# Optimization experiments

Hardware: AMD Instinct MI355X
Metric: run time of the kernel (lower is better)

The kernel has to match this reference:

```python
import jax, jax.numpy as jnp
import numpy as np

# Structure constants T[k, p, q] = sign such that (a (x) b)_k = sum_{p,q} T[k,p,q] a_p b_q,
# transcribed term-by-term from clifford_product_3d (Cl(3,0), metric +,+,+).
_TERMS = [
    (0,0,0, 1),(0,1,1, 1),(0,2,2, 1),(0,3,3, 1),(0,4,4,-1),(0,5,5,-1),(0,6,6,-1),(0,7,7,-1),
    (1,0,1, 1),(1,1,0, 1),(1,2,4,-1),(1,3,5, 1),(1,4,2, 1),(1,5,3,-1),(1,6,7,-1),(1,7,6,-1),
    (2,0,2, 1),(2,1,4, 1),(2,2,0, 1),(2,3,6,-1),(2,4,1,-1),(2,5,7, 1),(2,6,3, 1),(2,7,5,-1),
    (3,0,3, 1),(3,1,5,-1),(3,2,6, 1),(3,3,0, 1),(3,4,7,-1),(3,5,1,-1),(3,6,2,-1),(3,7,4, 1),
    (4,0,4, 1),(4,1,2, 1),(4,2,1,-1),(4,3,7, 1),(4,4,0, 1),(4,5,6,-1),(4,6,5, 1),(4,7,3,-1),
    (5,0,5, 1),(5,1,3,-1),(5,2,7, 1),(5,3,1, 1),(5,4,6, 1),(5,5,0, 1),(5,6,4,-1),(5,7,2,-1),
    (6,0,6, 1),(6,1,7,-1),(6,2,3,-1),(6,3,2, 1),(6,4,5,-1),(6,5,4, 1),(6,6,0, 1),(6,7,1, 1),
    (7,0,7, 1),(7,1,6, 1),(7,2,5,-1),(7,3,4, 1),(7,4,3, 1),(7,5,2,-1),(7,6,1, 1),(7,7,0, 1),
]

def _clifford_table():
    T = np.zeros((8, 8, 8), dtype=np.float32)
    for k, p, q, s in _TERMS:
        T[k, p, q] = s
    return jnp.asarray(T)

_T = _clifford_table()


def setup_inputs() -> dict:
    key = jax.random.key(0)
    k1, k2 = jax.random.split(key)
    C_in, C_out = 8, 8
    x = jax.random.normal(k1, (4096, 512, C_in, 8), dtype=jnp.float32)
    weight = jax.random.normal(k2, (C_out, C_in, 8), dtype=jnp.float32) * C_in ** (-0.5)
    bias = jnp.zeros((C_out, 8), dtype=jnp.float32)
    return {"x": x, "weight": weight, "bias": bias}


def reference(x, weight, bias):
    # out[..., o, k] = sum_i sum_{p,q} T[k,p,q] * weight[o,i,p] * x[..., i, q] + bias[o,k]
    # Contract weight with T first (tiny), then a single GEMM-like contraction over (i,q):
    # avoids the naive [..., C_out, C_in, 8] broadcast intermediate entirely.
    wT = jnp.einsum('kpq,oip->oikq', _T.astype(weight.dtype), weight)  # [C_out, C_in, 8, 8]
    out = jnp.einsum('oikq,biq->bok', wT, x.reshape(-1, *x.shape[-2:]))
    out = out.reshape(*x.shape[:-2], *out.shape[-2:])
    return out + bias
```

## Files before the change

kernel.cpp:

```cpp
#include <hip/hip_runtime.h>
#include <stdint.h>

__constant__ signed char QTAB[64] = {
    0,1,2,3,4,5,6,7,
    1,0,4,5,2,3,7,6,
    2,4,0,6,1,7,3,5,
    3,5,6,0,7,1,2,4,
    4,2,1,7,0,6,5,3,
    5,3,7,1,6,0,4,2,
    6,7,3,2,5,4,0,1,
    7,6,5,4,3,2,1,0};
__constant__ signed char SGN[64] = {
    1, 1, 1, 1,-1,-1,-1,-1,
    1, 1,-1, 1, 1,-1,-1,-1,
    1, 1, 1,-1,-1, 1, 1,-1,
    1,-1, 1, 1,-1,-1,-1, 1,
    1, 1,-1, 1, 1,-1, 1,-1,
    1,-1, 1, 1, 1, 1,-1,-1,
    1,-1,-1, 1,-1, 1, 1, 1,
    1, 1,-1, 1, 1,-1, 1, 1};

__global__ void clifford_prep(const float* __restrict__ weight,
                              float* __restrict__ W2) {
    int t = threadIdx.x;
    for (int e = t; e < 4096; e += 256) {
        int o = e >> 9, i = (e >> 6) & 7, k = (e >> 3) & 7, p = e & 7;
        int q = (int)QTAB[k * 8 + p];
        float s = (float)SGN[k * 8 + p];
        W2[((i * 8 + q) * 64) + (o * 8 + k)] = s * weight[(o * 8 + i) * 8 + p];
    }
}

#define LSTR 33

__global__ __launch_bounds__(256) void clifford_main(
    const float* __restrict__ x, const float* __restrict__ W,
    const float* __restrict__ bias, float* __restrict__ out, int nB) {
    __shared__ float lds[4][64 * LSTR];
    const int wave = threadIdx.x >> 6;
    const int lane = threadIdx.x & 63;
    float* Lw = lds[wave];
    const long long base = ((long long)blockIdx.x * 4 + wave) * 64;
    if (base >= nB) return;
    const float* xt = x + base * 64;
    float* ot = out + base * 64;
    const int r8 = lane >> 3;
    const int c8 = (lane & 7) * 4;

    float4 r0[8];
#pragma unroll
    for (int i = 0; i < 8; ++i)
        r0[i] = *(const float4*)(xt + (size_t)(r8 + 8 * i) * 64 + c8);
#pragma unroll
    for (int i = 0; i < 8; ++i) {
        int b = r8 + 8 * i;
        Lw[b * LSTR + c8 + 0] = r0[i].x;
        Lw[b * LSTR + c8 + 1] = r0[i].y;
        Lw[b * LSTR + c8 + 2] = r0[i].z;
        Lw[b * LSTR + c8 + 3] = r0[i].w;
    }

    float4 r1[8];
#pragma unroll
    for (int i = 0; i < 8; ++i)
        r1[i] = *(const float4*)(xt + (size_t)(r8 + 8 * i) * 64 + 32 + c8);

    float acc[64];
#pragma unroll
    for (int m = 0; m < 64; ++m) acc[m] = bias[m];

#pragma unroll 2
    for (int iq = 0; iq < 32; ++iq) {
        float xv = Lw[lane * LSTR + iq];
        const float* Wr = W + iq * 64;
#pragma unroll
        for (int m = 0; m < 64; ++m) acc[m] = fmaf(Wr[m], xv, acc[m]);
    }

#pragma unroll
    for (int i = 0; i < 8; ++i) {
        int b = r8 + 8 * i;
        Lw[b * LSTR + c8 + 0] = r1[i].x;
        Lw[b * LSTR + c8 + 1] = r1[i].y;
        Lw[b * LSTR + c8 + 2] = r1[i].z;
        Lw[b * LSTR + c8 + 3] = r1[i].w;
    }

#pragma unroll 2
    for (int iq = 0; iq < 32; ++iq) {
        float xv = Lw[lane * LSTR + iq];
        const float* Wr = W + (32 + iq) * 64;
#pragma unroll
        for (int m = 0; m < 64; ++m) acc[m] = fmaf(Wr[m], xv, acc[m]);
    }

#pragma unroll
    for (int mh = 0; mh < 2; ++mh) {
#pragma unroll
        for (int m = 0; m < 32; ++m) Lw[lane * LSTR + m] = acc[mh * 32 + m];
#pragma unroll
        for (int i = 0; i < 8; ++i) {
            int b = r8 + 8 * i;
            float4 v;
            v.x = Lw[b * LSTR + c8 + 0];
            v.y = Lw[b * LSTR + c8 + 1];
            v.z = Lw[b * LSTR + c8 + 2];
            v.w = Lw[b * LSTR + c8 + 3];
            *(float4*)(ot + (size_t)b * 64 + mh * 32 + c8) = v;
        }
    }
}

extern "C" void kernel_launch(void* const* d_in, const int* in_sizes, int n_in,
                              void* d_out, int out_size, void* d_ws,
                              size_t ws_size, hipStream_t stream) {
    const float* x = (const float*)d_in[0];
    const float* weight = (const float*)d_in[1];
    const float* bias = (const float*)d_in[2];
    float* out = (float*)d_out;
    float* W2 = (float*)d_ws;

    int nB = in_sizes[0] / 64;

    hipLaunchKernelGGL(clifford_prep, dim3(1), dim3(256), 0, stream, weight,
                       W2);
    int nTiles = (nB + 63) / 64;
    int blocks = (nTiles + 3) / 4;
    hipLaunchKernelGGL(clifford_main, dim3(blocks), dim3(256), 0, stream, x,
                       W2, bias, out, nB);
}
```

Baseline: 245.1 us.

## Make main kernel persistent with cross-tile prefetch of next x tile

Changes the grid from one wave per tile to a fixed 1024-block persistent grid where each wave loops over tiles with a stride. The first half of the next tile's input is loaded into registers during the second half of the current tile's compute, overlapping global loads with FMAs. Adds a launch_bounds occupancy hint of 4 blocks per CU. The kernel drops the partial-tile handling that used nB directly (nT = nB>>6), which is fine for the test size but assumes nB is a multiple of 64. The extra prefetch registers may raise register pressure.

```diff
diff --git a/kernel.cpp b/kernel.cpp
--- a/kernel.cpp
+++ b/kernel.cpp
@@ -32,81 +32,100 @@
 }
 
 #define LSTR 33
+#define NBLK 1024
 
-__global__ __launch_bounds__(256) void clifford_main(
+__global__ __launch_bounds__(256, 4) void clifford_main(
     const float* __restrict__ x, const float* __restrict__ W,
     const float* __restrict__ bias, float* __restrict__ out, int nB) {
     __shared__ float lds[4][64 * LSTR];
     const int wave = threadIdx.x >> 6;
     const int lane = threadIdx.x & 63;
     float* Lw = lds[wave];
-    const long long base = ((long long)blockIdx.x * 4 + wave) * 64;
-    if (base >= nB) return;
-    const float* xt = x + base * 64;
-    float* ot = out + base * 64;
+    const int nT = nB >> 6;
+    const int totw = NBLK * 4;
     const int r8 = lane >> 3;
     const int c8 = (lane & 7) * 4;
 
-    float4 r0[8];
+    int t = blockIdx.x * 4 + wave;
+    if (t >= nT) return;
+
+    float4 r0[8], r1[8];
+    {
+        const float* xt = x + (long long)t * 64 * 64;
 #pragma unroll
-    for (int i = 0; i < 8; ++i)
-        r0[i] = *(const float4*)(xt + (size_t)(r8 + 8 * i) * 64 + c8);
-#pragma unroll
-    for (int i = 0; i < 8; ++i) {
-        int b = r8 + 8 * i;
-        Lw[b * LSTR + c8 + 0] = r0[i].x;
-        Lw[b * LSTR + c8 + 1] = r0[i].y;
-        Lw[b * LSTR + c8 + 2] = r0[i].z;
-        Lw[b * LSTR + c8 + 3] = r0[i].w;
+        for (int i = 0; i < 8; ++i)
+            r0[i] = *(const float4*)(xt + (size_t)(r8 + 8 * i) * 64 + c8);
     }
 
-    float4 r1[8];
-#pragma unroll
-    for (int i = 0; i < 8; ++i)
-        r1[i] = *(const float4*)(xt + (size_t)(r8 + 8 * i) * 64 + 32 + c8);
+    for (; t < nT; t += totw) {
+        const float* xt = x + (long long)t * 64 * 64;
+        float* ot = out + (long long)t * 64 * 64;
 
-    float acc[64];
-#pragma unroll
-    for (int m = 0; m < 64; ++m) acc[m] = bias[m];
-
-#pragma unroll 2
-    for (int iq = 0; iq < 32; ++iq) {
-        float xv = Lw[lane * LSTR + iq];
-        const float* Wr = W + iq * 64;
-#pragma unroll
-        for (int m = 0; m < 64; ++m) acc[m] = fmaf(Wr[m], xv, acc[m]);
-    }
-
-#pragma unroll
-    for (int i = 0; i < 8; ++i) {
-        int b = r8 + 8 * i;
-        Lw[b * LSTR + c8 + 0] = r1[i].x;
-        Lw[b * LSTR + c8 + 1] = r1[i].y;
-        Lw[b * LSTR + c8 + 2] = r1[i].z;
-        Lw[b * LSTR + c8 + 3] = r1[i].w;
-    }
-
-#pragma unroll 2
-    for (int iq = 0; iq < 32; ++iq) {
-        float xv = Lw[lane * LSTR + iq];
-        const float* Wr = W + (32 + iq) * 64;
-#pragma unroll
-        for (int m = 0; m < 64; ++m) acc[m] = fmaf(Wr[m], xv, acc[m]);
-    }
-
-#pragma unroll
-    for (int mh = 0; mh < 2; ++mh) {
-#pragma unroll
-        for (int m = 0; m < 32; ++m) Lw[lane * LSTR + m] = acc[mh * 32 + m];
 #pragma unroll
         for (int i = 0; i < 8; ++i) {
             int b = r8 + 8 * i;
-            float4 v;
-            v.x = Lw[b * LSTR + c8 + 0];
-            v.y = Lw[b * LSTR + c8 + 1];
-            v.z = Lw[b * LSTR + c8 + 2];
-            v.w = Lw[b * LSTR + c8 + 3];
-            *(float4*)(ot + (size_t)b * 64 + mh * 32 + c8) = v;
+            Lw[b * LSTR + c8 + 0] = r0[i].x;
+            Lw[b * LSTR + c8 + 1] = r0[i].y;
+            Lw[b * LSTR + c8 + 2] = r0[i].z;
+            Lw[b * LSTR + c8 + 3] = r0[i].w;
+        }
+
+#pragma unroll
+        for (int i = 0; i < 8; ++i)
+            r1[i] = *(const float4*)(xt + (size_t)(r8 + 8 * i) * 64 + 32 + c8);
+
+        float acc[64];
+#pragma unroll
+        for (int m = 0; m < 64; ++m) acc[m] = bias[m];
+
+#pragma unroll 2
+        for (int iq = 0; iq < 32; ++iq) {
+            float xv = Lw[lane * LSTR + iq];
+            const float* Wr = W + iq * 64;
+#pragma unroll
+            for (int m = 0; m < 64; ++m) acc[m] = fmaf(Wr[m], xv, acc[m]);
+        }
+
+#pragma unroll
+        for (int i = 0; i < 8; ++i) {
+            int b = r8 + 8 * i;
+            Lw[b * LSTR + c8 + 0] = r1[i].x;
+            Lw[b * LSTR + c8 + 1] = r1[i].y;
+            Lw[b * LSTR + c8 + 2] = r1[i].z;
+            Lw[b * LSTR + c8 + 3] = r1[i].w;
+        }
+
+        int tn = t + totw;
+        if (tn < nT) {
+            const float* xn = x + (long long)tn * 64 * 64;
+#pragma unroll
+            for (int i = 0; i < 8; ++i)
+                r0[i] = *(const float4*)(xn + (size_t)(r8 + 8 * i) * 64 + c8);
+        }
+
+#pragma unroll 2
+        for (int iq = 0; iq < 32; ++iq) {
+            float xv = Lw[lane * LSTR + iq];
+            const float* Wr = W + (32 + iq) * 64;
+#pragma unroll
+            for (int m = 0; m < 64; ++m) acc[m] = fmaf(Wr[m], xv, acc[m]);
+        }
+
+#pragma unroll
+        for (int mh = 0; mh < 2; ++mh) {
+#pragma unroll
+            for (int m = 0; m < 32; ++m)
+                Lw[lane * LSTR + m] = acc[mh * 32 + m];
+#pragma unroll
+            for (int i = 0; i < 8; ++i) {
+                int b = r8 + 8 * i;
+                float4 v;
+                v.x = Lw[b * LSTR + c8 + 0];
+                v.y = Lw[b * LSTR + c8 + 1];
+                v.z = Lw[b * LSTR + c8 + 2];
+                v.w = Lw[b * LSTR + c8 + 3];
+                *(float4*)(ot + (size_t)b * 64 + mh * 32 + c8) = v;
+            }
         }
     }
 }
@@ -125,7 +144,8 @@
     hipLaunchKernelGGL(clifford_prep, dim3(1), dim3(256), 0, stream, weight,
                        W2);
     int nTiles = (nB + 63) / 64;
-    int blocks = (nTiles + 3) / 4;
+    int blocks = NBLK;
+    if (blocks * 4 > nTiles) blocks = (nTiles + 3) / 4;
     hipLaunchKernelGGL(clifford_main, dim3(blocks), dim3(256), 0, stream, x,
                        W2, bias, out, nB);
 }
```

Result: slower. 345.4 us (+40.9%).
